# Kernel optimization log

Hardware: AMD Instinct MI355X
Metric: run time of the kernel (lower is better)

Reference implementation:

```python
import jax, jax.numpy as jnp
import numpy as np

DIM = 960
N_HEADS = 15
N_KV_HEADS = 5
HEAD_DIM = DIM // N_HEADS  # 64
B, T = 4, 2048


def setup_inputs() -> dict:
    key = jax.random.key(0)
    ks = jax.random.split(key, 8)
    x = jax.random.normal(ks[0], (B, T, DIM), dtype=jnp.float32)
    # rotary tables as in llama: freqs = 1/theta^(2i/d), angles = t * freqs
    inv_freq = 1.0 / (10000.0 ** (jnp.arange(0, HEAD_DIM, 2, dtype=jnp.float32) / HEAD_DIM))
    t = jnp.arange(T, dtype=jnp.float32)
    ang = jnp.outer(t, inv_freq)  # [T, HEAD_DIM/2]
    freqs_cos = jnp.cos(ang)
    freqs_sin = jnp.sin(ang)
    scale = 0.02
    wq = jax.random.normal(ks[1], (DIM, N_HEADS * HEAD_DIM), dtype=jnp.float32) * scale
    wk = jax.random.normal(ks[2], (DIM, N_KV_HEADS * HEAD_DIM), dtype=jnp.float32) * scale
    wv = jax.random.normal(ks[3], (DIM, N_KV_HEADS * HEAD_DIM), dtype=jnp.float32) * scale
    wo = jax.random.normal(ks[4], (N_HEADS * HEAD_DIM, DIM), dtype=jnp.float32) * scale
    return {"x": x, "freqs_cos": freqs_cos, "freqs_sin": freqs_sin,
            "wq": wq, "wk": wk, "wv": wv, "wo": wo}


def _rope(u, cos, sin):
    # u: [B, T, H, D]; cos/sin: [T, D/2] -> broadcast [1, T, 1, D/2]
    ur = u[..., 0::2]
    ui = u[..., 1::2]
    c = cos[None, :, None, :]
    s = sin[None, :, None, :]
    out_r = ur * c - ui * s
    out_i = ur * s + ui * c
    return jnp.stack([out_r, out_i], axis=-1).reshape(u.shape)


def reference(x, freqs_cos, freqs_sin, wq, wk, wv, wo):
    Bx, Tx, _ = x.shape
    q = (x @ wq).reshape(Bx, Tx, N_HEADS, HEAD_DIM)
    k = (x @ wk).reshape(Bx, Tx, N_KV_HEADS, HEAD_DIM)
    v = (x @ wv).reshape(Bx, Tx, N_KV_HEADS, HEAD_DIM)
    q = _rope(q, freqs_cos, freqs_sin)
    k = _rope(k, freqs_cos, freqs_sin)
    # GQA: group queries per kv head, broadcast kv instead of repeating it
    G = N_HEADS // N_KV_HEADS  # 3
    qg = q.reshape(Bx, Tx, N_KV_HEADS, G, HEAD_DIM)
    scale = 1.0 / jnp.sqrt(jnp.asarray(HEAD_DIM, dtype=x.dtype))
    # scores: [B, KV, G, T(q), T(k)]
    scores = jnp.einsum('btkgd,bskd->bkgts', qg, k) * scale
    causal = jnp.tril(jnp.ones((Tx, Tx), dtype=bool))
    scores = jnp.where(causal[None, None, None, :, :], scores, jnp.finfo(scores.dtype).min)
    attn = jax.nn.softmax(scores, axis=-1)
    out = jnp.einsum('bkgts,bskd->btkgd', attn, v)
    out = out.reshape(Bx, Tx, N_HEADS * HEAD_DIM)
    return out @ wo
```

## Files before the change

### kernel.cpp

```cpp
#include <hip/hip_runtime.h>
#include <hip/hip_bf16.h>
#include <cmath>
#include <type_traits>

#define DIM  960
#define NH   15
#define NKV  5
#define HD   64
#define GQ   3
#define TSEQ 2048
#define BATCH 4
#define NQ   (NH * HD)
#define NKVD (NKV * HD)
#define NTOT (NQ + 2 * NKVD)
#define NTOT_PAD 1664
#define NO_PAD   1024

using bf16x8 = __attribute__((ext_vector_type(8))) short;
using f32x4  = __attribute__((ext_vector_type(4))) float;
using f32x16 = __attribute__((ext_vector_type(16))) float;

#define SCALE_L2E 0.18033688011112042f

static __device__ __forceinline__ ushort f2bf(float f) {
    __hip_bfloat16 h = __float2bfloat16(f);
    return *reinterpret_cast<ushort*>(&h);
}

static __device__ __forceinline__ float fast_exp2(float x) {
    return __builtin_amdgcn_exp2f(x);
}

typedef const __attribute__((address_space(1))) unsigned char* gp_t;
typedef __attribute__((address_space(3))) unsigned char* lp_t;

static __device__ __forceinline__ void gload_lds16(const void* g, void* l) {
    __builtin_amdgcn_global_load_lds((gp_t)g, (lp_t)l, 16, 0, 0);
}

static __device__ __forceinline__ int vpos(int t) {
    return (t & ~15) | ((( t >> 2) & 1) << 3) | (t & 3) | (((t >> 3) & 1) << 2);
}

__global__ __launch_bounds__(256)
void cvt_x(const float* __restrict__ x, ushort* __restrict__ xb, int n4)
{
    int i = blockIdx.x * blockDim.x + threadIdx.x;
    const int stride = gridDim.x * blockDim.x;
    for (; i < n4; i += stride) {
        float4 v = reinterpret_cast<const float4*>(x)[i];
        ushort4 o = {f2bf(v.x), f2bf(v.y), f2bf(v.z), f2bf(v.w)};
        reinterpret_cast<ushort4*>(xb)[i] = o;
    }
}

__global__ __launch_bounds__(256)
void transpose_wb(const float* __restrict__ wq, const float* __restrict__ wk,
                  const float* __restrict__ wv, const float* __restrict__ wo,
                  ushort* __restrict__ wqkvT, ushort* __restrict__ woT)
{
    __shared__ float tile[32][33];
    const float* src; ushort* dst; int ncols, dstoff;
    switch (blockIdx.z) {
        case 0:  src = wq; ncols = NQ;   dst = wqkvT; dstoff = 0;    break;
        case 1:  src = wk; ncols = NKVD; dst = wqkvT; dstoff = NQ;   break;
        case 2:  src = wv; ncols = NKVD; dst = wqkvT; dstoff = NQ + NKVD; break;
        default: src = wo; ncols = NQ;   dst = woT;   dstoff = 0;    break;
    }
    const int c0 = blockIdx.x * 32;
    if (c0 >= ncols) return;
    const int k0 = blockIdx.y * 32;
    const int tx = threadIdx.x & 31, ty = threadIdx.x >> 5;
    #pragma unroll
    for (int i = 0; i < 4; ++i)
        tile[ty * 4 + i][tx] = src[(size_t)(k0 + ty * 4 + i) * ncols + c0 + tx];
    __syncthreads();
    #pragma unroll
    for (int i = 0; i < 4; ++i) {
        const int c = c0 + ty * 4 + i;
        dst[(size_t)(dstoff + c) * DIM + k0 + tx] = f2bf(tile[tx][ty * 4 + i]);
    }
}

template<int EPI>
__global__ __launch_bounds__(256)
void gemm_mfma(const ushort* __restrict__ A,
               const ushort* __restrict__ BT,
               ushort* __restrict__ Cq, ushort* __restrict__ Ck,
               ushort* __restrict__ Cv, float* __restrict__ Cf,
               const float* __restrict__ fcos, const float* __restrict__ fsin,
               int K, int NT)
{
    __shared__ char lds[32 * 1024];

    const int tid  = threadIdx.x;
    const int wave = tid >> 6;
    const int lane = tid & 63;
    const int lr   = lane & 15;
    const int lg   = lane >> 4;
    const int wr   = wave >> 1;
    const int wc   = wave & 1;
    const int row0 = blockIdx.y * 128;
    const int col0 = blockIdx.x * 128;

    const int swz = ((lr >> 1) & 3) << 4;

    f32x4 acc[4][4];
    #pragma unroll
    for (int mi = 0; mi < 4; ++mi)
        #pragma unroll
        for (int ni = 0; ni < 4; ++ni)
            acc[mi][ni] = f32x4{0.f, 0.f, 0.f, 0.f};

    const int sr  = lane >> 2;
    const int scp = lane & 3;

    auto stage = [&](int t, int bufsel) {
        const int k0 = t * 32;
        char* Ab = lds + bufsel * 16384;
        char* Bb = Ab + 8192;
        #pragma unroll
        for (int i = 0; i < 2; ++i) {
            const int r0 = (wave * 2 + i) * 16;
            const int r  = r0 + sr;
            const int gc = scp ^ ((r >> 1) & 3);
            gload_lds16(A + (size_t)(row0 + r) * K + k0 + gc * 8, Ab + r0 * 64);
        }
        #pragma unroll
        for (int i = 0; i < 2; ++i) {
            const int r0 = (wave * 2 + i) * 16;
            const int r  = r0 + sr;
            const int gc = scp ^ ((r >> 1) & 3);
            gload_lds16(BT + (size_t)(col0 + r) * K + k0 + gc * 8, Bb + r0 * 64);
        }
    };

    auto compute = [&](int bufsel) {
        char* Ab = lds + bufsel * 16384;
        char* Bb = Ab + 8192;
        bf16x8 af[4], bfr[4];
        #pragma unroll
        for (int mi = 0; mi < 4; ++mi)
            af[mi] = *reinterpret_cast<const bf16x8*>(
                Ab + (wr * 64 + mi * 16 + lr) * 64 + (lg * 16 ^ swz));
        #pragma unroll
        for (int ni = 0; ni < 4; ++ni)
            bfr[ni] = *reinterpret_cast<const bf16x8*>(
                Bb + (wc * 64 + ni * 16 + lr) * 64 + (lg * 16 ^ swz));
        #pragma unroll
        for (int mi = 0; mi < 4; ++mi)
            #pragma unroll
            for (int ni = 0; ni < 4; ++ni)
                acc[mi][ni] = __builtin_amdgcn_mfma_f32_16x16x32_bf16(
                    af[mi], bfr[ni], acc[mi][ni], 0, 0, 0);
    };

    stage(0, 0);
    __syncthreads();
    for (int t = 0; t < NT; ++t) {
        if (t + 1 < NT) stage(t + 1, (t & 1) ^ 1);
        compute(t & 1);
        __syncthreads();
    }

    #pragma unroll
    for (int mi = 0; mi < 4; ++mi) {
        #pragma unroll
        for (int q = 0; q < 4; ++q) {
            const int row = row0 + wr * 64 + mi * 16 + lg * 4 + q;
            const int t   = row & (TSEQ - 1);
            const int bb  = row >> 11;
            #pragma unroll
            for (int ni = 0; ni < 4; ++ni) {
                const float vv = acc[mi][ni][q];
                const int col = col0 + wc * 64 + ni * 16 + lr;
                if (EPI == 0) {
                    if (col < DIM)
                        Cf[(size_t)row * DIM + col] = vv;
                } else {
                    const float pv = __shfl_xor(vv, 1);
                    if (col < NQ + NKVD) {
                        const int j = (col & (HD - 1)) >> 1;
                        const float c = fcos[t * 32 + j];
                        const float s = fsin[t * 32 + j];
                        const float ov = (lr & 1) ? (pv * s + vv * c)
                                                  : (vv * c - pv * s);
                        if (col < NQ) {
                            Cq[(size_t)row * NQ + col] = f2bf(ov * SCALE_L2E);
                        } else {
                            const int ck  = col - NQ;
                            const int kvh = ck >> 6, d = ck & 63;
                            Ck[((size_t)(bb * NKV + kvh) * TSEQ + t) * HD + d] = f2bf(ov);
                        }
                    } else if (col < NTOT) {
                        const int cv  = col - NQ - NKVD;
                        const int kvh = cv >> 6, d = cv & 63;
                        Cv[((size_t)(bb * NKV + kvh) * HD + d) * TSEQ + vpos(t)] = f2bf(vv);
                    }
                }
            }
        }
    }
}

__global__ __launch_bounds__(256)
void attn_mfma(const ushort* __restrict__ qh,
               const ushort* __restrict__ kh,
               const ushort* __restrict__ vh,
               ushort* __restrict__ ao)
{
    __shared__ char lds[32768];

    const int qa  = blockIdx.x;
    const int h   = blockIdx.y;
    const int b   = blockIdx.z;
    const int kvh = h / GQ;
    const int tid  = threadIdx.x;
    const int wave = tid >> 6;
    const int lane = tid & 63;
    const int ln31 = lane & 31;
    const int hi   = lane >> 5;
    const int hi4  = hi * 4;
    const int woff = wave * 32;

    const ushort* kbase = kh + (size_t)(b * NKV + kvh) * TSEQ * HD;
    const ushort* vbase = vh + (size_t)(b * NKV + kvh) * HD * TSEQ;

    const int srow8 = lane >> 3;
    const int sc    = lane & 7;

    auto stageKV = [&](int kt, int bufsel) {
        const int k0s = kt * 64;
        char* Kb = lds + bufsel * 8192;
        char* Vb = lds + 16384 + bufsel * 8192;
        #pragma unroll
        for (int i = 0; i < 2; ++i) {
            const int s16 = wave * 2 + i;
            const int row = s16 * 8 + srow8;
            const int cs  = sc ^ (row & 7);
            gload_lds16(kbase + (size_t)(k0s + row) * HD + cs * 8, Kb + s16 * 1024);
            gload_lds16(vbase + (size_t)row * TSEQ + k0s + cs * 8, Vb + s16 * 1024);
        }
    };

    #pragma unroll 1
    for (int seg = 0; seg < 2; ++seg) {
        const int qt   = seg ? 15 - qa : qa;
        const int q0   = qt * 128;
        const int qrow = q0 + woff + ln31;

        bf16x8 qf[4];
        {
            const ushort* qp = qh + ((size_t)(b * TSEQ) + qrow) * NQ + h * HD + hi * 8;
            #pragma unroll
            for (int s = 0; s < 4; ++s)
                qf[s] = *reinterpret_cast<const bf16x8*>(qp + s * 16);
        }

        f32x16 O0 = {}, O1 = {};
        float m = -INFINITY, l = 0.f;

        const int nkt = 2 * qt + 2;

        auto core = [&](auto diagc, int kt, int bufsel) {
            constexpr bool DIAG = decltype(diagc)::value;
            const int k0 = kt * 64;
            char* Kb = lds + bufsel * 8192;
            char* Vb = lds + 16384 + bufsel * 8192;

            if (DIAG && k0 > q0 + woff + 31) return;

            f32x16 acc0 = {}, acc1 = {};
            __builtin_amdgcn_s_setprio(1);
            #pragma unroll
            for (int s = 0; s < 4; ++s) {
                const int db0 = ln31 * 128 + (((s * 2 + hi) * 16) ^ ((ln31 & 7) << 4));
                bf16x8 kf0 = *reinterpret_cast<const bf16x8*>(Kb + db0);
                acc0 = __builtin_amdgcn_mfma_f32_32x32x16_bf16(kf0, qf[s], acc0, 0, 0, 0);
                bf16x8 kf1 = *reinterpret_cast<const bf16x8*>(Kb + 4096 + db0);
                acc1 = __builtin_amdgcn_mfma_f32_32x32x16_bf16(kf1, qf[s], acc1, 0, 0, 0);
            }
            __builtin_amdgcn_s_setprio(0);

            if (DIAG) {
                #pragma unroll
                for (int r = 0; r < 16; ++r) {
                    const int kc = k0 + ((r & 3) + 8 * (r >> 2)) + hi4;
                    if (kc > qrow)      acc0[r] = -INFINITY;
                    if (kc + 32 > qrow) acc1[r] = -INFINITY;
                }
            }
            float mt = -INFINITY;
            #pragma unroll
            for (int r = 0; r < 16; ++r) {
                mt = fmaxf(mt, acc0[r]);
                mt = fmaxf(mt, acc1[r]);
            }
            mt = fmaxf(mt, __shfl_xor(mt, 32));
            const float mn   = fmaxf(m, mt);
            const float corr = fast_exp2(m - mn);
            m = mn;

            float ls0 = 0.f, ls1 = 0.f;
            #pragma unroll
            for (int r = 0; r < 16; ++r) {
                const float p0 = fast_exp2(acc0[r] - mn);
                const float p1 = fast_exp2(acc1[r] - mn);
                acc0[r] = p0; acc1[r] = p1;
                ls0 += p0; ls1 += p1;
            }
            float ls = ls0 + ls1;
            ls += __shfl_xor(ls, 32);
            l = l * corr + ls;
            O0 = O0 * corr;
            O1 = O1 * corr;

            bf16x8 pa[4];
            #pragma unroll
            for (int ss = 0; ss < 4; ++ss) {
                #pragma unroll
                for (int j = 0; j < 8; ++j) {
                    const int r = 8 * (ss & 1) + j;
                    const float p = (ss < 2) ? acc0[r] : acc1[r];
                    pa[ss][j] = (short)f2bf(p);
                }
            }

            __builtin_amdgcn_s_setprio(1);
            #pragma unroll
            for (int ss = 0; ss < 4; ++ss) {
                const int db0 = ln31 * 128 + (((ss * 2 + hi) * 16) ^ ((ln31 & 7) << 4));
                bf16x8 vf0 = *reinterpret_cast<const bf16x8*>(Vb + db0);
                O0 = __builtin_amdgcn_mfma_f32_32x32x16_bf16(vf0, pa[ss], O0, 0, 0, 0);
                bf16x8 vf1 = *reinterpret_cast<const bf16x8*>(Vb + 4096 + db0);
                O1 = __builtin_amdgcn_mfma_f32_32x32x16_bf16(vf1, pa[ss], O1, 0, 0, 0);
            }
            __builtin_amdgcn_s_setprio(0);
        };

        stageKV(0, 0);
        __syncthreads();
        int buf = 0;
        #pragma unroll 1
        for (int kt = 0; kt < nkt; ++kt) {
            if (kt + 1 < nkt) stageKV(kt + 1, buf ^ 1);
            if (kt >= nkt - 2) core(std::integral_constant<bool, true>{}, kt, buf);
            else               core(std::integral_constant<bool, false>{}, kt, buf);
            __syncthreads();
            buf ^= 1;
        }

        const float inv = 1.f / l;
        ushort* aop = ao + ((size_t)(b * TSEQ) + qrow) * NQ + h * HD;
        #pragma unroll
        for (int g = 0; g < 4; ++g) {
            const int r0 = 4 * g;
            {
                const int dd = 8 * g + hi4;
                ushort4 st = {f2bf(O0[r0] * inv), f2bf(O0[r0 + 1] * inv),
                              f2bf(O0[r0 + 2] * inv), f2bf(O0[r0 + 3] * inv)};
                *reinterpret_cast<ushort4*>(aop + dd) = st;
            }
            {
                const int dd = 32 + 8 * g + hi4;
                ushort4 st = {f2bf(O1[r0] * inv), f2bf(O1[r0 + 1] * inv),
                              f2bf(O1[r0 + 2] * inv), f2bf(O1[r0 + 3] * inv)};
                *reinterpret_cast<ushort4*>(aop + dd) = st;
            }
        }
    }
}

extern "C" void kernel_launch(void* const* d_in, const int* in_sizes, int n_in,
                              void* d_out, int out_size, void* d_ws, size_t ws_size,
                              hipStream_t stream)
{
    const float* x    = (const float*)d_in[0];
    const float* fcos = (const float*)d_in[1];
    const float* fsin = (const float*)d_in[2];
    const float* wq   = (const float*)d_in[3];
    const float* wk   = (const float*)d_in[4];
    const float* wv   = (const float*)d_in[5];
    const float* wo   = (const float*)d_in[6];
    float* out = (float*)d_out;

    const int M = BATCH * TSEQ;

    ushort* xb    = (ushort*)d_ws;
    ushort* wqkvT = xb    + (size_t)M * DIM;
    ushort* woT   = wqkvT + (size_t)NTOT_PAD * DIM;
    ushort* qb    = woT   + (size_t)NO_PAD * DIM;
    ushort* kb    = qb    + (size_t)M * NQ;
    ushort* vt    = kb    + (size_t)M * NKVD;
    ushort* ao    = vt    + (size_t)M * NKVD;

    cvt_x<<<2048, 256, 0, stream>>>(x, xb, M * DIM / 4);
    transpose_wb<<<dim3(30, 30, 4), 256, 0, stream>>>(wq, wk, wv, wo, wqkvT, woT);

    gemm_mfma<1><<<dim3(NTOT_PAD / 128, M / 128), 256, 0, stream>>>(
        xb, wqkvT, qb, kb, vt, nullptr, fcos, fsin, DIM, DIM / 32);

    attn_mfma<<<dim3(8, NH, BATCH), 256, 0, stream>>>(qb, kb, vt, ao);

    gemm_mfma<0><<<dim3(NO_PAD / 128, M / 128), 256, 0, stream>>>(
        ao, woT, nullptr, nullptr, nullptr, out, nullptr, nullptr, NQ, NQ / 32);
}
```

Baseline: 250.4 us.

## Rewrite GEMMs as 512-thread 256-row tiles with deeper prefetch and staged MFMA

Replaces the 128x128 GEMM with a 512-thread kernel that computes 256xBN tiles. Global-to-LDS loads are issued two K-steps ahead with explicit vmcnt waits, and the MFMA work is split into four quadrants separated by barriers and s_setprio. Block IDs are remapped so neighbouring workgroups share operand tiles, aiming at better L2 reuse. QKV padding grows to 1792 to fit 256-wide tiles, which adds some wasted columns, and the grid gets coarser, which may hurt occupancy and wave balance.

```diff
diff --git a/kernel.cpp b/kernel.cpp
--- a/kernel.cpp
+++ b/kernel.cpp
@@ -13,7 +13,7 @@
 #define NQ   (NH * HD)
 #define NKVD (NKV * HD)
 #define NTOT (NQ + 2 * NKVD)
-#define NTOT_PAD 1664
+#define NTOT_PAD 1792
 #define NO_PAD   1024
 
 using bf16x8 = __attribute__((ext_vector_type(8))) short;
@@ -82,120 +82,195 @@
     }
 }
 
-template<int EPI>
-__global__ __launch_bounds__(256)
-void gemm_mfma(const ushort* __restrict__ A,
+template<int EPI, int BN>
+__global__ __launch_bounds__(512)
+void gemm_pipe(const ushort* __restrict__ A,
                const ushort* __restrict__ BT,
                ushort* __restrict__ Cq, ushort* __restrict__ Ck,
                ushort* __restrict__ Cv, float* __restrict__ Cf,
                const float* __restrict__ fcos, const float* __restrict__ fsin,
-               int K, int NT)
+               int nbx)
 {
-    __shared__ char lds[32 * 1024];
+    constexpr int KD  = 960;
+    constexpr int BK  = 32;
+    constexpr int NT  = 30;
+    constexpr int PWN = BN / 4;
+    constexpr int NF  = PWN / 32;
+    constexpr int ASZ = 256 * BK * 2;
+    constexpr int BSZ = BN * BK * 2;
+    constexpr int BUF = ASZ + BSZ;
+    constexpr int AR  = ASZ / 8192;
+    constexpr int BR  = BSZ / 8192;
+    constexpr int LPT = AR + BR;
+
+    __shared__ char lds[2 * BUF];
 
     const int tid  = threadIdx.x;
     const int wave = tid >> 6;
     const int lane = tid & 63;
     const int lr   = lane & 15;
     const int lg   = lane >> 4;
-    const int wr   = wave >> 1;
-    const int wc   = wave & 1;
-    const int row0 = blockIdx.y * 128;
-    const int col0 = blockIdx.x * 128;
-
-    const int swz = ((lr >> 1) & 3) << 4;
-
-    f32x4 acc[4][4];
+    const int wm   = wave >> 2;
+    const int wn   = wave & 3;
+
+    const int nwg = gridDim.x;
+    const int bid = blockIdx.x;
+    const int sb  = (bid & 7) * (nwg >> 3) + (bid >> 3);
+    const int bx  = sb % nbx;
+    const int by  = sb / nbx;
+    const int row0 = by * 256;
+    const int col0 = bx * BN;
+
+    f32x4 acc[2][2][4][NF];
     #pragma unroll
-    for (int mi = 0; mi < 4; ++mi)
-        #pragma unroll
-        for (int ni = 0; ni < 4; ++ni)
-            acc[mi][ni] = f32x4{0.f, 0.f, 0.f, 0.f};
-
-    const int sr  = lane >> 2;
-    const int scp = lane & 3;
-
-    auto stage = [&](int t, int bufsel) {
-        const int k0 = t * 32;
-        char* Ab = lds + bufsel * 16384;
-        char* Bb = Ab + 8192;
-        #pragma unroll
-        for (int i = 0; i < 2; ++i) {
-            const int r0 = (wave * 2 + i) * 16;
-            const int r  = r0 + sr;
-            const int gc = scp ^ ((r >> 1) & 3);
-            gload_lds16(A + (size_t)(row0 + r) * K + k0 + gc * 8, Ab + r0 * 64);
-        }
-        #pragma unroll
-        for (int i = 0; i < 2; ++i) {
-            const int r0 = (wave * 2 + i) * 16;
-            const int r  = r0 + sr;
-            const int gc = scp ^ ((r >> 1) & 3);
-            gload_lds16(BT + (size_t)(col0 + r) * K + k0 + gc * 8, Bb + r0 * 64);
+    for (int qm = 0; qm < 2; ++qm)
+        #pragma unroll
+        for (int qn = 0; qn < 2; ++qn)
+            #pragma unroll
+            for (int mi = 0; mi < 4; ++mi)
+                #pragma unroll
+                for (int ni = 0; ni < NF; ++ni)
+                    acc[qm][qn][mi][ni] = f32x4{0.f, 0.f, 0.f, 0.f};
+
+    auto stageA = [&](int t, int bsel) {
+        const int k0 = t * BK;
+        #pragma unroll
+        for (int rd = 0; rd < AR; ++rd) {
+            const int row = rd * 128 + wave * 16 + (lane >> 2);
+            const int gc  = (lane & 3) ^ ((row >> 1) & 3);
+            gload_lds16(A + (size_t)(row0 + row) * KD + k0 + gc * 8,
+                        lds + bsel * BUF + rd * 8192 + wave * 1024);
         }
     };
-
-    auto compute = [&](int bufsel) {
-        char* Ab = lds + bufsel * 16384;
-        char* Bb = Ab + 8192;
-        bf16x8 af[4], bfr[4];
+    auto stageB = [&](int t, int bsel) {
+        const int k0 = t * BK;
+        #pragma unroll
+        for (int rd = 0; rd < BR; ++rd) {
+            const int row = rd * 128 + wave * 16 + (lane >> 2);
+            const int gc  = (lane & 3) ^ ((row >> 1) & 3);
+            gload_lds16(BT + (size_t)(col0 + row) * KD + k0 + gc * 8,
+                        lds + bsel * BUF + ASZ + rd * 8192 + wave * 1024);
+        }
+    };
+
+    auto rdA = [&](int bsel, int qm, int mi) -> bf16x8 {
+        const int row = wm * 128 + qm * 64 + mi * 16 + lr;
+        const int ch  = lg ^ ((row >> 1) & 3);
+        return *reinterpret_cast<const bf16x8*>(lds + bsel * BUF + row * 64 + ch * 16);
+    };
+    auto rdB = [&](int bsel, int qn, int ni) -> bf16x8 {
+        const int row = wn * PWN + qn * (PWN / 2) + ni * 16 + lr;
+        const int ch  = lg ^ ((row >> 1) & 3);
+        return *reinterpret_cast<const bf16x8*>(lds + bsel * BUF + ASZ + row * 64 + ch * 16);
+    };
+
+    stageA(0, 0); stageB(0, 0);
+    stageA(1, 1); stageB(1, 1);
+
+    #pragma unroll 1
+    for (int t = 0; t < NT; ++t) {
+        const int bsel = t & 1;
+        if (t + 1 < NT) asm volatile("s_waitcnt vmcnt(%0)" :: "i"(LPT) : "memory");
+        else            asm volatile("s_waitcnt vmcnt(0)" ::: "memory");
+        __builtin_amdgcn_s_barrier();
+        __builtin_amdgcn_sched_barrier(0);
+
+        bf16x8 bfr[2][NF];
+        #pragma unroll
+        for (int qn = 0; qn < 2; ++qn)
+            #pragma unroll
+            for (int ni = 0; ni < NF; ++ni)
+                bfr[qn][ni] = rdB(bsel, qn, ni);
+        bf16x8 af[4];
+        #pragma unroll
+        for (int mi = 0; mi < 4; ++mi) af[mi] = rdA(bsel, 0, mi);
+        asm volatile("s_waitcnt lgkmcnt(0)" ::: "memory");
+        __builtin_amdgcn_sched_barrier(0);
+        __builtin_amdgcn_s_setprio(1);
         #pragma unroll
         for (int mi = 0; mi < 4; ++mi)
-            af[mi] = *reinterpret_cast<const bf16x8*>(
-                Ab + (wr * 64 + mi * 16 + lr) * 64 + (lg * 16 ^ swz));
-        #pragma unroll
-        for (int ni = 0; ni < 4; ++ni)
-            bfr[ni] = *reinterpret_cast<const bf16x8*>(
-                Bb + (wc * 64 + ni * 16 + lr) * 64 + (lg * 16 ^ swz));
+            #pragma unroll
+            for (int ni = 0; ni < NF; ++ni)
+                acc[0][0][mi][ni] = __builtin_amdgcn_mfma_f32_16x16x32_bf16(
+                    af[mi], bfr[0][ni], acc[0][0][mi][ni], 0, 0, 0);
+        __builtin_amdgcn_s_setprio(0);
+        __builtin_amdgcn_s_barrier();
+
+        bf16x8 an[4];
+        #pragma unroll
+        for (int mi = 0; mi < 4; ++mi) an[mi] = rdA(bsel, 1, mi);
+        asm volatile("s_waitcnt lgkmcnt(0)" ::: "memory");
+        __builtin_amdgcn_sched_barrier(0);
+        __builtin_amdgcn_s_setprio(1);
         #pragma unroll
         for (int mi = 0; mi < 4; ++mi)
             #pragma unroll
-            for (int ni = 0; ni < 4; ++ni)
-                acc[mi][ni] = __builtin_amdgcn_mfma_f32_16x16x32_bf16(
-                    af[mi], bfr[ni], acc[mi][ni], 0, 0, 0);
-    };
-
-    stage(0, 0);
-    __syncthreads();
-    for (int t = 0; t < NT; ++t) {
-        if (t + 1 < NT) stage(t + 1, (t & 1) ^ 1);
-        compute(t & 1);
-        __syncthreads();
+            for (int ni = 0; ni < NF; ++ni)
+                acc[0][1][mi][ni] = __builtin_amdgcn_mfma_f32_16x16x32_bf16(
+                    af[mi], bfr[1][ni], acc[0][1][mi][ni], 0, 0, 0);
+        __builtin_amdgcn_s_setprio(0);
+        __builtin_amdgcn_s_barrier();
+
+        if (t + 2 < NT) { stageA(t + 2, bsel); stageB(t + 2, bsel); }
+        __builtin_amdgcn_s_setprio(1);
+        #pragma unroll
+        for (int mi = 0; mi < 4; ++mi)
+            #pragma unroll
+            for (int ni = 0; ni < NF; ++ni)
+                acc[1][0][mi][ni] = __builtin_amdgcn_mfma_f32_16x16x32_bf16(
+                    an[mi], bfr[0][ni], acc[1][0][mi][ni], 0, 0, 0);
+        __builtin_amdgcn_s_setprio(0);
+        __builtin_amdgcn_s_barrier();
+
+        __builtin_amdgcn_s_setprio(1);
+        #pragma unroll
+        for (int mi = 0; mi < 4; ++mi)
+            #pragma unroll
+            for (int ni = 0; ni < NF; ++ni)
+                acc[1][1][mi][ni] = __builtin_amdgcn_mfma_f32_16x16x32_bf16(
+                    an[mi], bfr[1][ni], acc[1][1][mi][ni], 0, 0, 0);
+        __builtin_amdgcn_s_setprio(0);
     }
 
     #pragma unroll
-    for (int mi = 0; mi < 4; ++mi) {
-        #pragma unroll
-        for (int q = 0; q < 4; ++q) {
-            const int row = row0 + wr * 64 + mi * 16 + lg * 4 + q;
-            const int t   = row & (TSEQ - 1);
-            const int bb  = row >> 11;
-            #pragma unroll
-            for (int ni = 0; ni < 4; ++ni) {
-                const float vv = acc[mi][ni][q];
-                const int col = col0 + wc * 64 + ni * 16 + lr;
-                if (EPI == 0) {
-                    if (col < DIM)
-                        Cf[(size_t)row * DIM + col] = vv;
-                } else {
-                    const float pv = __shfl_xor(vv, 1);
-                    if (col < NQ + NKVD) {
-                        const int j = (col & (HD - 1)) >> 1;
-                        const float c = fcos[t * 32 + j];
-                        const float s = fsin[t * 32 + j];
-                        const float ov = (lr & 1) ? (pv * s + vv * c)
-                                                  : (vv * c - pv * s);
-                        if (col < NQ) {
-                            Cq[(size_t)row * NQ + col] = f2bf(ov * SCALE_L2E);
+    for (int qm = 0; qm < 2; ++qm) {
+        #pragma unroll
+        for (int qn = 0; qn < 2; ++qn) {
+            #pragma unroll
+            for (int mi = 0; mi < 4; ++mi) {
+                #pragma unroll
+                for (int ni = 0; ni < NF; ++ni) {
+                    #pragma unroll
+                    for (int q = 0; q < 4; ++q) {
+                        const int row = row0 + wm * 128 + qm * 64 + mi * 16 + lg * 4 + q;
+                        const int col = col0 + wn * PWN + qn * (PWN / 2) + ni * 16 + lr;
+                        const int t   = row & (TSEQ - 1);
+                        const int bb  = row >> 11;
+                        const float vv = acc[qm][qn][mi][ni][q];
+                        if (EPI == 0) {
+                            if (col < DIM)
+                                Cf[(size_t)row * DIM + col] = vv;
                         } else {
-                            const int ck  = col - NQ;
-                            const int kvh = ck >> 6, d = ck & 63;
-                            Ck[((size_t)(bb * NKV + kvh) * TSEQ + t) * HD + d] = f2bf(ov);
+                            const float pv = __shfl_xor(vv, 1);
+                            if (col < NQ + NKVD) {
+                                const int j = (col & (HD - 1)) >> 1;
+                                const float c = fcos[t * 32 + j];
+                                const float s = fsin[t * 32 + j];
+                                const float ov = (lr & 1) ? (pv * s + vv * c)
+                                                          : (vv * c - pv * s);
+                                if (col < NQ) {
+                                    Cq[(size_t)row * NQ + col] = f2bf(ov * SCALE_L2E);
+                                } else {
+                                    const int ck  = col - NQ;
+                                    const int kvh = ck >> 6, d = ck & 63;
+                                    Ck[((size_t)(bb * NKV + kvh) * TSEQ + t) * HD + d] = f2bf(ov);
+                                }
+                            } else if (col < NTOT) {
+                                const int cv  = col - NQ - NKVD;
+                                const int kvh = cv >> 6, d = cv & 63;
+                                Cv[((size_t)(bb * NKV + kvh) * HD + d) * TSEQ + vpos(t)] = f2bf(vv);
+                            }
                         }
-                    } else if (col < NTOT) {
-                        const int cv  = col - NQ - NKVD;
-                        const int kvh = cv >> 6, d = cv & 63;
-                        Cv[((size_t)(bb * NKV + kvh) * HD + d) * TSEQ + vpos(t)] = f2bf(vv);
                     }
                 }
             }
@@ -397,11 +472,11 @@
     cvt_x<<<2048, 256, 0, stream>>>(x, xb, M * DIM / 4);
     transpose_wb<<<dim3(30, 30, 4), 256, 0, stream>>>(wq, wk, wv, wo, wqkvT, woT);
 
-    gemm_mfma<1><<<dim3(NTOT_PAD / 128, M / 128), 256, 0, stream>>>(
-        xb, wqkvT, qb, kb, vt, nullptr, fcos, fsin, DIM, DIM / 32);
+    gemm_pipe<1, 256><<<dim3((NTOT_PAD / 256) * (M / 256)), 512, 0, stream>>>(
+        xb, wqkvT, qb, kb, vt, nullptr, fcos, fsin, NTOT_PAD / 256);
 
     attn_mfma<<<dim3(8, NH, BATCH), 256, 0, stream>>>(qb, kb, vt, ao);
 
-    gemm_mfma<0><<<dim3(NO_PAD / 128, M / 128), 256, 0, stream>>>(
-        ao, woT, nullptr, nullptr, nullptr, out, nullptr, nullptr, NQ, NQ / 32);
-}
+    gemm_pipe<0, 128><<<dim3((NO_PAD / 128) * (M / 256)), 512, 0, stream>>>(
+        ao, woT, nullptr, nullptr, nullptr, out, nullptr, nullptr, NO_PAD / 128);
+}
```

Result: faster. 242.2 us (-3.3%).
